# Optimization experiments

Measured on AMD Instinct MI355X. Metric: run time of the kernel, lower is better.

Reference implementation:

```python
import jax, jax.numpy as jnp
import numpy as np

EPS = 1e-5

def _bn(x, g, b, m, v):
    # eval-mode batchnorm, NCHW, per-channel params
    inv = g / jnp.sqrt(v + EPS)
    return x * inv[None, :, None, None] + (b - m * inv)[None, :, None, None]

def setup_inputs() -> dict:
    key = jax.random.key(0)
    ks = jax.random.split(key, 16)
    C = 64
    x = jax.random.normal(ks[0], (8, C, 64, 64), dtype=jnp.float32)
    w1 = jax.random.normal(ks[1], (C, C, 1, 1), dtype=jnp.float32) * 0.1
    w2 = jax.random.normal(ks[2], (C, 1, 3, 3), dtype=jnp.float32) * 0.1
    w3 = jax.random.normal(ks[3], (C, C, 1, 1), dtype=jnp.float32) * 0.1
    def bn_params(k):
        k1, k2, k3, k4 = jax.random.split(k, 4)
        return (jax.random.uniform(k1, (C,)) + 0.5,
                jax.random.normal(k2, (C,)) * 0.1,
                jax.random.normal(k3, (C,)) * 0.1,
                jax.random.uniform(k4, (C,)) + 0.5)
    g1, b1, m1, v1 = bn_params(ks[4])
    g2, b2, m2, v2 = bn_params(ks[5])
    g3, b3, m3, v3 = bn_params(ks[6])
    return {"x": x, "w1": w1, "bn1_g": g1, "bn1_b": b1, "bn1_m": m1, "bn1_v": v1,
            "w2": w2, "bn2_g": g2, "bn2_b": b2, "bn2_m": m2, "bn2_v": v2,
            "w3": w3, "bn3_g": g3, "bn3_b": b3, "bn3_m": m3, "bn3_v": v3}

def reference(x, w1, bn1_g, bn1_b, bn1_m, bn1_v,
              w2, bn2_g, bn2_b, bn2_m, bn2_v,
              w3, bn3_g, bn3_b, bn3_m, bn3_v):
    B, c, h, w = x.shape
    N = h * w
    # conv1 (1x1) + BN + ReLU -> V
    v = jnp.einsum('bchw,oc->bohw', x, w1[:, :, 0, 0])
    v = jax.nn.relu(_bn(v, bn1_g, bn1_b, bn1_m, bn1_v))
    # attention over spatial positions: Q=K=x, single head, dim=c
    Q = x.reshape(B, c, N)          # bdn
    V = v.reshape(B, c, N)          # bdm
    scores = jnp.einsum('bdn,bdm->bnm', Q, Q) / (c ** 0.5)  # [B,N,N]
    prob = jax.nn.softmax(scores, axis=-1)
    out = jnp.einsum('bnm,bdm->bdn', prob, V).reshape(B, c, h, w)
    # depthwise conv + BN + ReLU
    out = jax.lax.conv_general_dilated(
        out, w2, window_strides=(1, 1), padding='SAME',
        dimension_numbers=('NCHW', 'OIHW', 'NCHW'), feature_group_count=c)
    out = jax.nn.relu(_bn(out, bn2_g, bn2_b, bn2_m, bn2_v))
    # pointwise conv + BN
    out = jnp.einsum('bchw,oc->bohw', out, w3[:, :, 0, 0])
    out = _bn(out, bn3_g, bn3_b, bn3_m, bn3_v)
    # residual (stride==1 and in_size==out_size)
    return out + x
```

## Files before the change

kernel.cpp:

```cpp
#include <hip/hip_runtime.h>
#include <stdint.h>

typedef __attribute__((ext_vector_type(8)))  short s16x8;
typedef __attribute__((ext_vector_type(16))) float f32x16;
typedef __attribute__((ext_vector_type(2)))  unsigned u32x2;

union CvtI4 { int4 i; s16x8 s; };
union CvtU4 { uint4 u; s16x8 s; };

__device__ __forceinline__ unsigned f2bf(float f) {
    union { float f; unsigned u; } v; v.f = f;
    return (v.u + 0x7fffu + ((v.u >> 16) & 1u)) >> 16;
}

__device__ __forceinline__ unsigned packbf(float lo, float hi) {
    union { float f; unsigned u; } a0, a1;
    a0.f = lo; a1.f = hi;
    return __builtin_amdgcn_perm(a1.u + 0x8000u, a0.u + 0x8000u, 0x07060302u);
}

__global__ __launch_bounds__(256) void k_prep(
    const float* __restrict__ x, const float* __restrict__ w1,
    const float* __restrict__ g1, const float* __restrict__ b1,
    const float* __restrict__ m1, const float* __restrict__ v1,
    unsigned short* __restrict__ xT, unsigned short* __restrict__ vbf)
{
    __shared__ float X[64 * 65];
    const int b    = blockIdx.x >> 7;
    const int n0   = ((blockIdx.x >> 1) & 63) << 6;
    const int half = blockIdx.x & 1;
    const int tid  = threadIdx.x;
    const float QS = 0.42466090014400953f;

    {
        const int r = tid >> 6, nn = tid & 63;
        const float* xb = x + (size_t)b * 262144 + n0 + nn;
#pragma unroll
        for (int cc = 0; cc < 16; ++cc) {
            int c = cc * 4 + r;
            X[c * 65 + nn] = xb[(size_t)c * 4096];
        }
    }
    __syncthreads();

    {
        const int n8 = tid >> 3, c8 = tid & 7;
        const int n = (half << 5) + n8;
        unsigned u[4];
#pragma unroll
        for (int j = 0; j < 4; ++j) {
            unsigned lo = f2bf(X[(c8 * 8 + 2 * j) * 65 + n] * QS);
            unsigned hi = f2bf(X[(c8 * 8 + 2 * j + 1) * 65 + n] * QS);
            u[j] = lo | (hi << 16);
        }
        uint4 pk; pk.x = u[0]; pk.y = u[1]; pk.z = u[2]; pk.w = u[3];
        *(uint4*)(xT + (((size_t)((b << 12) + n0 + n)) << 6) + (c8 << 3)) = pk;
    }

    {
        const int n = tid & 63, og = tid >> 6;
        float rX[64];
#pragma unroll
        for (int c = 0; c < 64; ++c) rX[c] = X[c * 65 + n];
        unsigned short* vb = vbf + (((size_t)(b << 6)) << 12) + n0 + n;
#pragma unroll 2
        for (int oo = 0; oo < 8; ++oo) {
            int o = (half << 5) + og * 8 + oo;
            float inv = g1[o] * rsqrtf(v1[o] + 1e-5f);
            float sh  = b1[o] - m1[o] * inv;
            float acc = 0.f;
#pragma unroll
            for (int c = 0; c < 64; ++c) acc = fmaf(w1[o * 64 + c], rX[c], acc);
            vb[(size_t)o << 12] = (unsigned short)f2bf(fmaxf(fmaf(acc, inv, sh), 0.f));
        }
    }
}

__global__ __launch_bounds__(512, 4) void k_attn(
    const unsigned short* __restrict__ xT, const unsigned short* __restrict__ vbf,
    unsigned short* __restrict__ outO)
{
    __shared__ __align__(16) unsigned short Kl[2][2][64 * 64];
    __shared__ __align__(16) unsigned short Vl[2][2][64 * 64];

    const int b    = blockIdx.x & 7;
    const int qgrp = blockIdx.x >> 3;
    const int tid  = threadIdx.x;
    const int w = tid >> 6, lane = tid & 63;
    const int l31 = lane & 31, half = lane >> 5;
    const int qbase = qgrp << 6;
    const int qd = w & 3, par = w >> 2;
    const int s = qd & 1;
    const int t = qd >> 1;

    s16x8 Bq[4];
    {
        const unsigned short* qr = xT +
            (((size_t)((b << 12) + qbase + (t << 5) + l31)) << 6) + (half << 3);
#pragma unroll
        for (int kk = 0; kk < 4; ++kk) {
            CvtI4 c; c.i = *(const int4*)(qr + (kk << 4));
            Bq[kk] = c.s;
        }
    }

    const int pt = tid >> 8;
    const int sr = (tid >> 3) & 31;
    const int sc = tid & 7;
    const unsigned short* kBase = xT  + ((size_t)b << 18) + (sr << 6) + (sc << 3);
    const unsigned short* vBase = vbf + ((size_t)b << 18) + ((size_t)sr << 12) + (sc << 3);
    const int kx  = (sc ^ (sr & 7)) << 3;
    const int d0  = (sr << 6) + kx;
    const int d1  = ((sr + 32) << 6) + kx;

    int4 kpA, kpB, vpA, vpB;

    {
        int4 a0 = *(const int4*)(kBase + ((size_t)pt << 12));
        int4 a1 = *(const int4*)(kBase + ((size_t)pt << 12) + (32 << 6));
        int4 b0 = *(const int4*)(vBase + (pt << 6));
        int4 b1v = *(const int4*)(vBase + ((size_t)32 << 12) + (pt << 6));
        unsigned short* Kd = &Kl[0][pt][0];
        unsigned short* Vd = &Vl[0][pt][0];
        *(int4*)(Kd + d0) = a0; *(int4*)(Kd + d1) = a1;
        *(int4*)(Vd + d0) = b0; *(int4*)(Vd + d1) = b1v;
        const int t1 = 2 + pt;
        kpA = *(const int4*)(kBase + ((size_t)t1 << 12));
        kpB = *(const int4*)(kBase + ((size_t)t1 << 12) + (32 << 6));
        vpA = *(const int4*)(vBase + (t1 << 6));
        vpB = *(const int4*)(vBase + ((size_t)32 << 12) + (t1 << 6));
    }
    __syncthreads();

    f32x16 O[2];
#pragma unroll
    for (int dl = 0; dl < 2; ++dl)
#pragma unroll
        for (int r = 0; r < 16; ++r) O[dl][r] = 0.f;
    float rs = 0.f;

    const int km = (s << 5) + l31;

    for (int p = 0; p < 32; ++p) {
        {
            unsigned short* Kd = &Kl[(p + 1) & 1][pt][0];
            unsigned short* Vd = &Vl[(p + 1) & 1][pt][0];
            *(int4*)(Kd + d0) = kpA; *(int4*)(Kd + d1) = kpB;
            *(int4*)(Vd + d0) = vpA; *(int4*)(Vd + d1) = vpB;
        }
        {
            int tn = ((p + 2) << 1) + pt; if (tn > 63) tn = 63;
            kpA = *(const int4*)(kBase + ((size_t)tn << 12));
            kpB = *(const int4*)(kBase + ((size_t)tn << 12) + (32 << 6));
            vpA = *(const int4*)(vBase + (tn << 6));
            vpB = *(const int4*)(vBase + ((size_t)32 << 12) + (tn << 6));
        }

        const unsigned short* Kb = &Kl[p & 1][par][0];
        s16x8 Ak[4];
#pragma unroll
        for (int kk = 0; kk < 4; ++kk)
            Ak[kk] = *(const s16x8*)(Kb + (km << 6) + ((((kk << 1) + half) ^ (km & 7)) << 3));
        f32x16 S = {0.f,0.f,0.f,0.f,0.f,0.f,0.f,0.f,0.f,0.f,0.f,0.f,0.f,0.f,0.f,0.f};
        __builtin_amdgcn_s_setprio(1);
        S = __builtin_amdgcn_mfma_f32_32x32x16_bf16(Ak[0], Bq[0], S, 0, 0, 0);
        S = __builtin_amdgcn_mfma_f32_32x32x16_bf16(Ak[1], Bq[1], S, 0, 0, 0);
        S = __builtin_amdgcn_mfma_f32_32x32x16_bf16(Ak[2], Bq[2], S, 0, 0, 0);
        S = __builtin_amdgcn_mfma_f32_32x32x16_bf16(Ak[3], Bq[3], S, 0, 0, 0);
        __builtin_amdgcn_s_setprio(0);

        uint2 G[4];
#pragma unroll
        for (int q = 0; q < 4; ++q) {
            float p0 = __builtin_amdgcn_exp2f(S[4*q+0]);
            float p1 = __builtin_amdgcn_exp2f(S[4*q+1]);
            float p2 = __builtin_amdgcn_exp2f(S[4*q+2]);
            float p3 = __builtin_amdgcn_exp2f(S[4*q+3]);
            rs += (p0 + p1) + (p2 + p3);
            G[q].x = packbf(p0, p1);
            G[q].y = packbf(p2, p3);
        }

        const unsigned short* Vb = &Vl[p & 1][par][0];
        __builtin_amdgcn_s_setprio(1);
#pragma unroll
        for (int ksl = 0; ksl < 2; ++ksl) {
            u32x2 r0 = __builtin_amdgcn_permlane32_swap(G[2*ksl].x, G[2*ksl+1].x, false, false);
            u32x2 r1 = __builtin_amdgcn_permlane32_swap(G[2*ksl].y, G[2*ksl+1].y, false, false);
            CvtU4 ac;
            ac.u.x = r0.x;
            ac.u.y = r1.x;
            ac.u.z = r0.y;
            ac.u.w = r1.y;
            const s16x8 Ap = ac.s;
#pragma unroll
            for (int dl = 0; dl < 2; ++dl) {
                const int drow = (dl << 5) + l31;
                const int cch = (s << 2) + (ksl << 1) + half;
                const s16x8 Bv = *(const s16x8*)(Vb + (drow << 6) + ((cch ^ (drow & 7)) << 3));
                O[dl] = __builtin_amdgcn_mfma_f32_32x32x16_bf16(Ap, Bv, O[dl], 0, 0, 0);
            }
        }
        __builtin_amdgcn_s_setprio(0);

        __syncthreads();
    }

    float* scr  = (float*)&Kl[0][0][0];
    float* scr2 = (float*)&Vl[0][0][0];
    float* rsL  = scr2 + 4096;
    float* dnm  = rsL + 256;

    rs += __shfl_xor(rs, 32);
    if (half == 0) rsL[(w << 5) + l31] = rs;
    if (par == 1) {
#pragma unroll
        for (int dl = 0; dl < 2; ++dl)
#pragma unroll
            for (int r = 0; r < 16; ++r)
                scr[((((qd << 1) + dl)) << 10) + (r << 6) + lane] = O[dl][r];
    }
    __syncthreads();

    if (tid < 64) {
        int tt = tid >> 5, n = tid & 31;
        dnm[tid] = (rsL[((tt << 1) << 5) + n] + rsL[(((tt << 1) + 1) << 5) + n]) +
                   (rsL[(((tt << 1) + 4) << 5) + n] + rsL[(((tt << 1) + 5) << 5) + n]);
    }
    if (par == 0) {
#pragma unroll
        for (int dl = 0; dl < 2; ++dl)
#pragma unroll
            for (int r = 0; r < 16; ++r)
                O[dl][r] += scr[((((qd << 1) + dl)) << 10) + (r << 6) + lane];
        if (s == 1) {
#pragma unroll
            for (int dl = 0; dl < 2; ++dl)
#pragma unroll
                for (int r = 0; r < 16; ++r)
                    scr2[((((t << 1) + dl)) << 10) + (r << 6) + lane] = O[dl][r];
        }
    }
    __syncthreads();

    if (par == 0 && s == 0) {
        const int nb = (b << 12) + qbase;
#pragma unroll
        for (int r = 0; r < 16; ++r) {
            int rowoff = (r & 3) + ((r >> 2) << 3) + (half << 2);
            int n = (t << 5) + rowoff;
            float inv = 1.f / dnm[n];
#pragma unroll
            for (int dl = 0; dl < 2; ++dl) {
                float o = O[dl][r] + scr2[((((t << 1) + dl)) << 10) + (r << 6) + lane];
                outO[((size_t)(nb + n) << 6) + (dl << 5) + l31] =
                    (unsigned short)f2bf(o * inv);
            }
        }
    }
}

__global__ __launch_bounds__(256) void k_post(
    const unsigned short* __restrict__ Obase,
    const float* __restrict__ x,
    const float* __restrict__ w2,
    const float* __restrict__ g2, const float* __restrict__ b2,
    const float* __restrict__ m2, const float* __restrict__ v2,
    const float* __restrict__ w3,
    const float* __restrict__ g3, const float* __restrict__ b3,
    const float* __restrict__ m3, const float* __restrict__ v3,
    float* __restrict__ out)
{
    __shared__ float W[3][64 * 66];
    __shared__ float T2[64 * 66];

    const int b = blockIdx.x >> 6;
    const int h = blockIdx.x & 63;
    const int tid = threadIdx.x;

#pragma unroll
    for (int r = 0; r < 3; ++r) {
        int hh = h + r - 1;
        if (hh >= 0 && hh <= 63) {
#pragma unroll
            for (int i = 0; i < 2; ++i) {
                int lin = (i << 8) + tid;
                int w = lin >> 3, cg = lin & 7;
                size_t npos = (size_t)((b << 12) + (hh << 6) + w);
                uint4 v = *(const uint4*)(Obase + (npos << 6) + (cg << 3));
                float* Wd = &W[r][w * 66 + (cg << 3)];
                union { float f; unsigned u; } t;
                t.u = v.x << 16;         Wd[0] = t.f;
                t.u = v.x & 0xFFFF0000u; Wd[1] = t.f;
                t.u = v.y << 16;         Wd[2] = t.f;
                t.u = v.y & 0xFFFF0000u; Wd[3] = t.f;
                t.u = v.z << 16;         Wd[4] = t.f;
                t.u = v.z & 0xFFFF0000u; Wd[5] = t.f;
                t.u = v.w << 16;         Wd[6] = t.f;
                t.u = v.w & 0xFFFF0000u; Wd[7] = t.f;
            }
        } else {
#pragma unroll
            for (int i = 0; i < 2; ++i) {
                int lin = (i << 8) + tid;
                float* Wd = &W[r][(lin >> 3) * 66 + ((lin & 7) << 3)];
#pragma unroll
                for (int j = 0; j < 8; ++j) Wd[j] = 0.f;
            }
        }
    }
    __syncthreads();

    const int w = tid & 63, cq = tid >> 6;
    float t16[16];
#pragma unroll
    for (int i = 0; i < 16; ++i) t16[i] = 0.f;

#pragma unroll
    for (int ky = 0; ky < 3; ++ky) {
#pragma unroll
        for (int kx = 0; kx < 3; ++kx) {
            int ww = w + kx - 1;
            if (ww < 0 || ww > 63) continue;
            const int k = ky * 3 + kx;
            const float* Wr = &W[ky][ww * 66 + (cq << 4)];
#pragma unroll
            for (int i = 0; i < 4; ++i) {
                float4 a = *(const float4*)(Wr + (i << 2));
                int c = (cq << 4) + (i << 2);
                t16[i * 4 + 0] = fmaf(w2[(c + 0) * 9 + k], a.x, t16[i * 4 + 0]);
                t16[i * 4 + 1] = fmaf(w2[(c + 1) * 9 + k], a.y, t16[i * 4 + 1]);
                t16[i * 4 + 2] = fmaf(w2[(c + 2) * 9 + k], a.z, t16[i * 4 + 2]);
                t16[i * 4 + 3] = fmaf(w2[(c + 3) * 9 + k], a.w, t16[i * 4 + 3]);
            }
        }
    }
#pragma unroll
    for (int i = 0; i < 16; ++i) {
        int c = (cq << 4) + i;
        float inv = g2[c] * rsqrtf(v2[c] + 1e-5f);
        float sh  = b2[c] - m2[c] * inv;
        T2[w * 66 + c] = fmaxf(fmaf(t16[i], inv, sh), 0.f);
    }
    __syncthreads();

    float rT[64];
#pragma unroll
    for (int c4 = 0; c4 < 16; ++c4)
        *(float4*)&rT[c4 << 2] = *(const float4*)&T2[w * 66 + (c4 << 2)];

    const int hw = (h << 6) + w;
#pragma unroll 2
    for (int oo = 0; oo < 16; ++oo) {
        int o = (cq << 4) + oo;
        float inv = g3[o] * rsqrtf(v3[o] + 1e-5f);
        float sh  = b3[o] - m3[o] * inv;
        float acc = 0.f;
#pragma unroll
        for (int c = 0; c < 64; ++c) acc = fmaf(w3[o * 64 + c], rT[c], acc);
        size_t idx = (((size_t)((b << 6) + o)) << 12) + hw;
        out[idx] = fmaf(acc, inv, sh) + x[idx];
    }
}

extern "C" void kernel_launch(void* const* d_in, const int* in_sizes, int n_in,
                              void* d_out, int out_size, void* d_ws, size_t ws_size,
                              hipStream_t stream)
{
    const float* x  = (const float*)d_in[0];
    const float* w1 = (const float*)d_in[1];
    const float* g1 = (const float*)d_in[2];
    const float* b1 = (const float*)d_in[3];
    const float* m1 = (const float*)d_in[4];
    const float* v1 = (const float*)d_in[5];
    const float* w2 = (const float*)d_in[6];
    const float* g2 = (const float*)d_in[7];
    const float* b2 = (const float*)d_in[8];
    const float* m2 = (const float*)d_in[9];
    const float* v2 = (const float*)d_in[10];
    const float* w3 = (const float*)d_in[11];
    const float* g3 = (const float*)d_in[12];
    const float* b3 = (const float*)d_in[13];
    const float* m3 = (const float*)d_in[14];
    const float* v3 = (const float*)d_in[15];
    float* out = (float*)d_out;

    unsigned short* xT  = (unsigned short*)d_ws;
    unsigned short* vbf = xT + (size_t)8 * 4096 * 64;
    unsigned short* Obase = (unsigned short*)((char*)d_ws + (8u << 20));

    k_prep<<<1024, 256, 0, stream>>>(x, w1, g1, b1, m1, v1, xT, vbf);
    k_attn<<<512, 512, 0, stream>>>(xT, vbf, Obase);
    k_post<<<512, 256, 0, stream>>>(Obase, x, w2, g2, b2, m2, v2,
                                    w3, g3, b3, m3, v3, out);
}
```

Before: 185.5 us.

## Software-pipeline PV MFMA one tile behind QK MFMA in attention loop

Restructures the attention inner loop so the P·V MFMAs for tile p-1 are issued before the QK^T MFMAs of tile p, using the packed probabilities and V fragments held in registers from the previous iteration. An epilogue after the loop handles the final tile, and zero-initialised carries make the first iteration harmless. The aim is to overlap the exp/pack softmax work with independent matrix work and hide the MFMA dependency latency. In exchange it holds extra registers for the carried fragments, which may reduce occupancy.

```diff
diff --git a/kernel.cpp b/kernel.cpp
--- a/kernel.cpp
+++ b/kernel.cpp
@@ -139,6 +139,16 @@
         for (int r = 0; r < 16; ++r) O[dl][r] = 0.f;
     float rs = 0.f;
 
+    uint2 Gh[4];
+    s16x8 Bvh[4];
+    {
+        const s16x8 z = {0, 0, 0, 0, 0, 0, 0, 0};
+#pragma unroll
+        for (int q = 0; q < 4; ++q) { Gh[q].x = 0u; Gh[q].y = 0u; }
+#pragma unroll
+        for (int j = 0; j < 4; ++j) Bvh[j] = z;
+    }
+
     const int km = (s << 5) + l31;
 
     for (int p = 0; p < 32; ++p) {
@@ -161,15 +171,26 @@
 #pragma unroll
         for (int kk = 0; kk < 4; ++kk)
             Ak[kk] = *(const s16x8*)(Kb + (km << 6) + ((((kk << 1) + half) ^ (km & 7)) << 3));
+
+        __builtin_amdgcn_s_setprio(1);
+#pragma unroll
+        for (int ksl = 0; ksl < 2; ++ksl) {
+            u32x2 r0 = __builtin_amdgcn_permlane32_swap(Gh[2*ksl].x, Gh[2*ksl+1].x, false, false);
+            u32x2 r1 = __builtin_amdgcn_permlane32_swap(Gh[2*ksl].y, Gh[2*ksl+1].y, false, false);
+            CvtU4 ac;
+            ac.u.x = r0.x; ac.u.y = r1.x; ac.u.z = r0.y; ac.u.w = r1.y;
+            const s16x8 Ap = ac.s;
+            O[0] = __builtin_amdgcn_mfma_f32_32x32x16_bf16(Ap, Bvh[2*ksl + 0], O[0], 0, 0, 0);
+            O[1] = __builtin_amdgcn_mfma_f32_32x32x16_bf16(Ap, Bvh[2*ksl + 1], O[1], 0, 0, 0);
+        }
+
         f32x16 S = {0.f,0.f,0.f,0.f,0.f,0.f,0.f,0.f,0.f,0.f,0.f,0.f,0.f,0.f,0.f,0.f};
-        __builtin_amdgcn_s_setprio(1);
         S = __builtin_amdgcn_mfma_f32_32x32x16_bf16(Ak[0], Bq[0], S, 0, 0, 0);
         S = __builtin_amdgcn_mfma_f32_32x32x16_bf16(Ak[1], Bq[1], S, 0, 0, 0);
         S = __builtin_amdgcn_mfma_f32_32x32x16_bf16(Ak[2], Bq[2], S, 0, 0, 0);
         S = __builtin_amdgcn_mfma_f32_32x32x16_bf16(Ak[3], Bq[3], S, 0, 0, 0);
         __builtin_amdgcn_s_setprio(0);
 
-        uint2 G[4];
 #pragma unroll
         for (int q = 0; q < 4; ++q) {
             float p0 = __builtin_amdgcn_exp2f(S[4*q+0]);
@@ -177,33 +198,35 @@
             float p2 = __builtin_amdgcn_exp2f(S[4*q+2]);
             float p3 = __builtin_amdgcn_exp2f(S[4*q+3]);
             rs += (p0 + p1) + (p2 + p3);
-            G[q].x = packbf(p0, p1);
-            G[q].y = packbf(p2, p3);
-        }
-
-        const unsigned short* Vb = &Vl[p & 1][par][0];
-        __builtin_amdgcn_s_setprio(1);
-#pragma unroll
-        for (int ksl = 0; ksl < 2; ++ksl) {
-            u32x2 r0 = __builtin_amdgcn_permlane32_swap(G[2*ksl].x, G[2*ksl+1].x, false, false);
-            u32x2 r1 = __builtin_amdgcn_permlane32_swap(G[2*ksl].y, G[2*ksl+1].y, false, false);
-            CvtU4 ac;
-            ac.u.x = r0.x;
-            ac.u.y = r1.x;
-            ac.u.z = r0.y;
-            ac.u.w = r1.y;
-            const s16x8 Ap = ac.s;
-#pragma unroll
-            for (int dl = 0; dl < 2; ++dl) {
-                const int drow = (dl << 5) + l31;
-                const int cch = (s << 2) + (ksl << 1) + half;
-                const s16x8 Bv = *(const s16x8*)(Vb + (drow << 6) + ((cch ^ (drow & 7)) << 3));
-                O[dl] = __builtin_amdgcn_mfma_f32_32x32x16_bf16(Ap, Bv, O[dl], 0, 0, 0);
-            }
-        }
-        __builtin_amdgcn_s_setprio(0);
+            Gh[q].x = packbf(p0, p1);
+            Gh[q].y = packbf(p2, p3);
+        }
+
+        {
+            const unsigned short* Vb = &Vl[p & 1][par][0];
+#pragma unroll
+            for (int ksl = 0; ksl < 2; ++ksl)
+#pragma unroll
+                for (int dl = 0; dl < 2; ++dl) {
+                    const int drow = (dl << 5) + l31;
+                    const int cch = (s << 2) + (ksl << 1) + half;
+                    Bvh[2*ksl + dl] =
+                        *(const s16x8*)(Vb + (drow << 6) + ((cch ^ (drow & 7)) << 3));
+                }
+        }
 
         __syncthreads();
+    }
+
+#pragma unroll
+    for (int ksl = 0; ksl < 2; ++ksl) {
+        u32x2 r0 = __builtin_amdgcn_permlane32_swap(Gh[2*ksl].x, Gh[2*ksl+1].x, false, false);
+        u32x2 r1 = __builtin_amdgcn_permlane32_swap(Gh[2*ksl].y, Gh[2*ksl+1].y, false, false);
+        CvtU4 ac;
+        ac.u.x = r0.x; ac.u.y = r1.x; ac.u.z = r0.y; ac.u.w = r1.y;
+        const s16x8 Ap = ac.s;
+        O[0] = __builtin_amdgcn_mfma_f32_32x32x16_bf16(Ap, Bvh[2*ksl + 0], O[0], 0, 0, 0);
+        O[1] = __builtin_amdgcn_mfma_f32_32x32x16_bf16(Ap, Bvh[2*ksl + 1], O[1], 0, 0, 0);
     }
 
     float* scr  = (float*)&Kl[0][0][0];
```

Measured after the change: 210.1 us. +13.2%, slower.

## Split post-processing kernel into half-row tiles with halo for more blocks

Applied to the files above, without the earlier changes.

The depthwise+pointwise post kernel now processes half an image row (32 columns) per block with a one-column halo, doubling the grid to 1024 blocks. Each thread handles 8 channels instead of 16 for the depthwise stage and 8 output channels for the pointwise stage. This raises parallelism and lowers shared memory and registers per block, but adds redundant halo loads and re-reads w3 per block. The post kernel is likely a small share of total time next to attention.

```diff
diff --git a/kernel.cpp b/kernel.cpp
--- a/kernel.cpp
+++ b/kernel.cpp
@@ -271,88 +271,86 @@
     const float* __restrict__ m3, const float* __restrict__ v3,
     float* __restrict__ out)
 {
-    __shared__ float W[3][64 * 66];
-    __shared__ float T2[64 * 66];
-
-    const int b = blockIdx.x >> 6;
-    const int h = blockIdx.x & 63;
+    __shared__ float W[3][34 * 66];
+    __shared__ float T2[32 * 66];
+
+    const int b  = blockIdx.x >> 7;
+    const int h  = (blockIdx.x >> 1) & 63;
+    const int wh = blockIdx.x & 1;
+    const int wbase = wh << 5;
     const int tid = threadIdx.x;
 
 #pragma unroll
     for (int r = 0; r < 3; ++r) {
         int hh = h + r - 1;
-        if (hh >= 0 && hh <= 63) {
+#pragma unroll
+        for (int i = 0; i < 2; ++i) {
+            int lin = (i << 8) + tid;
+            if (lin < 272) {
+                int wl = lin >> 3, cg = lin & 7;
+                int wg = wbase + wl - 1;
+                float* Wd = &W[r][wl * 66 + (cg << 3)];
+                if (hh >= 0 && hh <= 63 && wg >= 0 && wg <= 63) {
+                    size_t npos = (size_t)((b << 12) + (hh << 6) + wg);
+                    uint4 v = *(const uint4*)(Obase + (npos << 6) + (cg << 3));
+                    union { float f; unsigned u; } t;
+                    t.u = v.x << 16;         Wd[0] = t.f;
+                    t.u = v.x & 0xFFFF0000u; Wd[1] = t.f;
+                    t.u = v.y << 16;         Wd[2] = t.f;
+                    t.u = v.y & 0xFFFF0000u; Wd[3] = t.f;
+                    t.u = v.z << 16;         Wd[4] = t.f;
+                    t.u = v.z & 0xFFFF0000u; Wd[5] = t.f;
+                    t.u = v.w << 16;         Wd[6] = t.f;
+                    t.u = v.w & 0xFFFF0000u; Wd[7] = t.f;
+                } else {
+#pragma unroll
+                    for (int j = 0; j < 8; ++j) Wd[j] = 0.f;
+                }
+            }
+        }
+    }
+    __syncthreads();
+
+    const int w32 = tid & 31, cq = tid >> 5;
+    float t8[8];
+#pragma unroll
+    for (int i = 0; i < 8; ++i) t8[i] = 0.f;
+
+#pragma unroll
+    for (int ky = 0; ky < 3; ++ky) {
+#pragma unroll
+        for (int kx = 0; kx < 3; ++kx) {
+            const int k = ky * 3 + kx;
+            const float* Wr = &W[ky][(w32 + kx) * 66 + (cq << 3)];
 #pragma unroll
             for (int i = 0; i < 2; ++i) {
-                int lin = (i << 8) + tid;
-                int w = lin >> 3, cg = lin & 7;
-                size_t npos = (size_t)((b << 12) + (hh << 6) + w);
-                uint4 v = *(const uint4*)(Obase + (npos << 6) + (cg << 3));
-                float* Wd = &W[r][w * 66 + (cg << 3)];
-                union { float f; unsigned u; } t;
-                t.u = v.x << 16;         Wd[0] = t.f;
-                t.u = v.x & 0xFFFF0000u; Wd[1] = t.f;
-                t.u = v.y << 16;         Wd[2] = t.f;
-                t.u = v.y & 0xFFFF0000u; Wd[3] = t.f;
-                t.u = v.z << 16;         Wd[4] = t.f;
-                t.u = v.z & 0xFFFF0000u; Wd[5] = t.f;
-                t.u = v.w << 16;         Wd[6] = t.f;
-                t.u = v.w & 0xFFFF0000u; Wd[7] = t.f;
+                float4 a = *(const float4*)(Wr + (i << 2));
+                int c = (cq << 3) + (i << 2);
+                t8[i * 4 + 0] = fmaf(w2[(c + 0) * 9 + k], a.x, t8[i * 4 + 0]);
+                t8[i * 4 + 1] = fmaf(w2[(c + 1) * 9 + k], a.y, t8[i * 4 + 1]);
+                t8[i * 4 + 2] = fmaf(w2[(c + 2) * 9 + k], a.z, t8[i * 4 + 2]);
+                t8[i * 4 + 3] = fmaf(w2[(c + 3) * 9 + k], a.w, t8[i * 4 + 3]);
             }
-        } else {
-#pragma unroll
-            for (int i = 0; i < 2; ++i) {
-                int lin = (i << 8) + tid;
-                float* Wd = &W[r][(lin >> 3) * 66 + ((lin & 7) << 3)];
-#pragma unroll
-                for (int j = 0; j < 8; ++j) Wd[j] = 0.f;
-            }
-        }
-    }
-    __syncthreads();
-
-    const int w = tid & 63, cq = tid >> 6;
-    float t16[16];
-#pragma unroll
-    for (int i = 0; i < 16; ++i) t16[i] = 0.f;
-
-#pragma unroll
-    for (int ky = 0; ky < 3; ++ky) {
-#pragma unroll
-        for (int kx = 0; kx < 3; ++kx) {
-            int ww = w + kx - 1;
-            if (ww < 0 || ww > 63) continue;
-            const int k = ky * 3 + kx;
-            const float* Wr = &W[ky][ww * 66 + (cq << 4)];
-#pragma unroll
-            for (int i = 0; i < 4; ++i) {
-                float4 a = *(const float4*)(Wr + (i << 2));
-                int c = (cq << 4) + (i << 2);
-                t16[i * 4 + 0] = fmaf(w2[(c + 0) * 9 + k], a.x, t16[i * 4 + 0]);
-                t16[i * 4 + 1] = fmaf(w2[(c + 1) * 9 + k], a.y, t16[i * 4 + 1]);
-                t16[i * 4 + 2] = fmaf(w2[(c + 2) * 9 + k], a.z, t16[i * 4 + 2]);
-                t16[i * 4 + 3] = fmaf(w2[(c + 3) * 9 + k], a.w, t16[i * 4 + 3]);
-            }
-        }
-    }
-#pragma unroll
-    for (int i = 0; i < 16; ++i) {
-        int c = (cq << 4) + i;
+        }
+    }
+#pragma unroll
+    for (int i = 0; i < 8; ++i) {
+        int c = (cq << 3) + i;
         float inv = g2[c] * rsqrtf(v2[c] + 1e-5f);
         float sh  = b2[c] - m2[c] * inv;
-        T2[w * 66 + c] = fmaxf(fmaf(t16[i], inv, sh), 0.f);
+        T2[w32 * 66 + c] = fmaxf(fmaf(t8[i], inv, sh), 0.f);
     }
     __syncthreads();
 
     float rT[64];
 #pragma unroll
     for (int c4 = 0; c4 < 16; ++c4)
-        *(float4*)&rT[c4 << 2] = *(const float4*)&T2[w * 66 + (c4 << 2)];
-
-    const int hw = (h << 6) + w;
+        *(float4*)&rT[c4 << 2] = *(const float4*)&T2[w32 * 66 + (c4 << 2)];
+
+    const int hw = (h << 6) + wbase + w32;
 #pragma unroll 2
-    for (int oo = 0; oo < 16; ++oo) {
-        int o = (cq << 4) + oo;
+    for (int oo = 0; oo < 8; ++oo) {
+        int o = (cq << 3) + oo;
         float inv = g3[o] * rsqrtf(v3[o] + 1e-5f);
         float sh  = b3[o] - m3[o] * inv;
         float acc = 0.f;
@@ -391,6 +389,6 @@
 
     k_prep<<<1024, 256, 0, stream>>>(x, w1, g1, b1, m1, v1, xT, vbf);
     k_attn<<<512, 512, 0, stream>>>(xT, vbf, Obase);
-    k_post<<<512, 256, 0, stream>>>(Obase, x, w2, g2, b2, m2, v2,
-                                    w3, g3, b3, m3, v3, out);
-}
+    k_post<<<1024, 256, 0, stream>>>(Obase, x, w2, g2, b2, m2, v2,
+                                     w3, g3, b3, m3, v3, out);
+}
```

Measured after the change: 184.8 us. About the same (-0.4%).
